# Optimization experiments

Hardware: AMD Instinct MI355X
Metric: run time of the kernel (lower is better)

## Reference

```python
import jax, jax.numpy as jnp
import numpy as np

N = 20000   # nodes
E = 320000  # edges (before self loops)
B = 32      # graphs in batch
H = 4       # heads
C = 64      # per-head channels
NEG_SLOPE = 0.2


def setup_inputs() -> dict:
    key = jax.random.key(0)
    ks = jax.random.split(key, 16)
    x = jax.random.normal(ks[0], (N, 62), jnp.float32)
    pos = jax.random.uniform(ks[1], (N, 2), jnp.float32)
    edge_index = jax.random.randint(ks[2], (2, E), 0, N, jnp.int64)
    batch = jnp.sort(jax.random.randint(ks[3], (N,), 0, B, jnp.int64))
    def glorot(k, shape):
        fan = shape[0] + shape[-1]
        return jax.random.normal(k, shape, jnp.float32) * jnp.sqrt(2.0 / fan)
    # GAT layer 1: in 64 -> H*C = 256
    W1 = glorot(ks[4], (64, H * C))
    a_src1 = glorot(ks[5], (H, C))
    a_dst1 = glorot(ks[6], (H, C))
    b1 = jnp.zeros((H * C,), jnp.float32)
    # GAT layer 2: in 256 -> 256
    W2 = glorot(ks[7], (H * C, H * C))
    a_src2 = glorot(ks[8], (H, C))
    a_dst2 = glorot(ks[9], (H, C))
    b2 = jnp.zeros((H * C,), jnp.float32)
    # linear tail 256 -> 128 -> 10
    lw1 = glorot(ks[10], (H * C, 128))
    lb1 = jnp.zeros((128,), jnp.float32)
    lw2 = glorot(ks[11], (128, 10))
    lb2 = jnp.zeros((10,), jnp.float32)
    return {"x": x, "pos": pos, "edge_index": edge_index, "batch": batch,
            "W1": W1, "a_src1": a_src1, "a_dst1": a_dst1, "b1": b1,
            "W2": W2, "a_src2": a_src2, "a_dst2": a_dst2, "b2": b2,
            "lw1": lw1, "lb1": lb1, "lw2": lw2, "lb2": lb2}


def gat_layer(x, src, dst, W, a_src, a_dst, b):
    # x: [N, F_in] -> h: [N, H, C]
    h = (x @ W).reshape(N, H, C)
    alpha_s = jnp.einsum('nhc,hc->nh', h, a_src)  # [N,H]
    alpha_d = jnp.einsum('nhc,hc->nh', h, a_dst)
    e = alpha_s[src] + alpha_d[dst]               # [E',H]
    e = jax.nn.leaky_relu(e, NEG_SLOPE)
    # softmax over incoming edges per destination node
    emax = jax.ops.segment_max(e, dst, num_segments=N)  # every node has a self loop
    p = jnp.exp(e - emax[dst])
    denom = jax.ops.segment_sum(p, dst, num_segments=N)
    alpha = p / (denom[dst] + 1e-16)              # [E',H]
    msg = h[src] * alpha[..., None]               # [E',H,C] gather + weight
    out = jax.ops.segment_sum(msg, dst, num_segments=N)  # scatter-add
    return out.reshape(N, H * C) + b


def reference(x, pos, edge_index, batch, W1, a_src1, a_dst1, b1,
              W2, a_src2, a_dst2, b2, lw1, lb1, lw2, lb2):
    out = jnp.concatenate([pos, x], axis=1)       # [N, 64]
    loop = jnp.arange(N, dtype=edge_index.dtype)
    src = jnp.concatenate([edge_index[0], loop])  # add self loops (PyG default)
    dst = jnp.concatenate([edge_index[1], loop])
    out = gat_layer(out, src, dst, W1, a_src1, a_dst1, b1)
    out = gat_layer(out, src, dst, W2, a_src2, a_dst2, b2)
    # global mean pool per graph
    sums = jax.ops.segment_sum(out, batch, num_segments=B)
    cnt = jax.ops.segment_sum(jnp.ones((N, 1), out.dtype), batch, num_segments=B)
    out = sums / jnp.maximum(cnt, 1.0)            # [B, 256]
    # dropout(p=0.2) is identity in eval mode
    out = jax.nn.relu(out @ lw1 + lb1)
    out = jax.nn.relu(out @ lw2 + lb2)            # relu after every linear, incl. last (faithful)
    return out
```

## Files before the change

kernel.cpp:

```cpp
#include <hip/hip_runtime.h>
#include <hip/hip_bf16.h>
#include <math.h>

#define N_NODES 20000
#define N_EDGES 320000
#define N_EDGES_SL (N_EDGES + N_NODES)
#define NB 32
#define NH 4
#define NC 64
#define HC 256
#define POOL_CH 20
#define DCAP 64

typedef short s16x8 __attribute__((ext_vector_type(8)));
typedef unsigned short u16x8 __attribute__((ext_vector_type(8)));
typedef float f32x4 __attribute__((ext_vector_type(4)));

__device__ __forceinline__ float bf2f(ushort u) {
    union { unsigned int i; float f; } v; v.i = ((unsigned int)u) << 16; return v.f;
}
__device__ __forceinline__ ushort f2bf(float f) {
    union { float f; unsigned int i; } v; v.f = f;
    unsigned int u = v.i;
    unsigned int r = (u + 0x7FFFu + ((u >> 16) & 1u)) >> 16;
    return (ushort)r;
}

#define PB_CONCAT 5000
#define PB_TCONV1 64
#define PB_TCONV2 256
#define PB_FILL   ((N_EDGES_SL + 255) / 256)
__global__ __launch_bounds__(256) void prep_kernel(const float* __restrict__ x,
                                                   const float* __restrict__ pos,
                                                   ushort* __restrict__ x0,
                                                   const float* __restrict__ W1,
                                                   ushort* __restrict__ Wt1,
                                                   const float* __restrict__ W2,
                                                   ushort* __restrict__ Wt2,
                                                   const int* __restrict__ ei,
                                                   int* __restrict__ fillc,
                                                   int* __restrict__ srclist,
                                                   const int* __restrict__ batch,
                                                   int* __restrict__ gstart) {
    int blk = blockIdx.x;
    if (blk < PB_CONCAT) {
        int i = blk * 256 + threadIdx.x;
        int n = i >> 6, j = i & 63;
        float v = (j < 2) ? pos[n * 2 + j] : x[n * 62 + (j - 2)];
        x0[i] = f2bf(v);
    } else if (blk < PB_CONCAT + PB_TCONV1) {
        int i = (blk - PB_CONCAT) * 256 + threadIdx.x;
        int n = i >> 6, k = i & 63;
        Wt1[i] = f2bf(W1[k * 256 + n]);
    } else if (blk < PB_CONCAT + PB_TCONV1 + PB_TCONV2) {
        int i = (blk - PB_CONCAT - PB_TCONV1) * 256 + threadIdx.x;
        int n = i >> 8, k = i & 255;
        Wt2[i] = f2bf(W2[k * 256 + n]);
    } else if (blk < PB_CONCAT + PB_TCONV1 + PB_TCONV2 + PB_FILL) {
        int i = (blk - PB_CONCAT - PB_TCONV1 - PB_TCONV2) * 256 + threadIdx.x;
        if (i >= N_EDGES_SL) return;
        int src, dst;
        if (i < N_EDGES) { src = ei[i]; dst = ei[N_EDGES + i]; }
        else             { src = i - N_EDGES; dst = src; }
        int slot = atomicAdd(&fillc[dst], 1);
        if (slot < DCAP) srclist[dst * DCAP + slot] = src;
    } else {
        int t = threadIdx.x;
        if (t > NB) return;
        int lo = 0, hi = N_NODES;
        while (lo < hi) {
            int mid = (lo + hi) >> 1;
            if (batch[mid] < t) lo = mid + 1; else hi = mid;
        }
        gstart[t] = lo;
    }
}

template<int K, int KC>
__global__ __launch_bounds__(256) void mfma_gemm(const ushort* __restrict__ A,
                                                 const ushort* __restrict__ Bt,
                                                 ushort* __restrict__ C,
                                                 const float* __restrict__ a_src,
                                                 const float* __restrict__ a_dst,
                                                 float* __restrict__ asb,
                                                 float* __restrict__ adb,
                                                 int M) {
    constexpr int KP = KC + 8;
    __shared__ __align__(16) ushort As[64 * KP];
    __shared__ __align__(16) ushort Bs[128 * KP];
    int tid = threadIdx.x;
    int row0 = blockIdx.y * 64, col0 = blockIdx.x * 128;
    int wave = tid >> 6, lane = tid & 63;
    int mm = lane & 15, quad = lane >> 4;
    f32x4 acc[8] = {};

    for (int kc0 = 0; kc0 < K; kc0 += KC) {
        if (kc0) __syncthreads();
        constexpr int ITER_A = (64 * KC) / 2048;
        constexpr int ITER_B = (128 * KC) / 2048;
#pragma unroll
        for (int it = 0; it < ITER_A; ++it) {
            int f = it * 2048 + tid * 8;
            int r = f / KC, k = f - r * KC;
            uint4 av = make_uint4(0u, 0u, 0u, 0u);
            if (row0 + r < M) av = *(const uint4*)&A[(size_t)(row0 + r) * K + kc0 + k];
            *(uint4*)&As[r * KP + k] = av;
        }
#pragma unroll
        for (int it = 0; it < ITER_B; ++it) {
            int f = it * 2048 + tid * 8;
            int r = f / KC, k = f - r * KC;
            uint4 bv = *(const uint4*)&Bt[(size_t)(col0 + r) * K + kc0 + k];
            *(uint4*)&Bs[r * KP + k] = bv;
        }
        __syncthreads();
#pragma unroll
        for (int kt = 0; kt < KC / 32; ++kt) {
            s16x8 a = *(const s16x8*)&As[(wave * 16 + mm) * KP + kt * 32 + quad * 8];
#pragma unroll
            for (int nt = 0; nt < 8; ++nt) {
                s16x8 b = *(const s16x8*)&Bs[(nt * 16 + mm) * KP + kt * 32 + quad * 8];
                acc[nt] = __builtin_amdgcn_mfma_f32_16x16x32_bf16(a, b, acc[nt], 0, 0, 0);
            }
        }
    }
#pragma unroll
    for (int r = 0; r < 4; ++r) {
        int gr = row0 + wave * 16 + quad * 4 + r;
        bool ok = gr < M;
        float s1a = 0.f, s2a = 0.f, s1b = 0.f, s2b = 0.f;
#pragma unroll
        for (int nt = 0; nt < 8; ++nt) {
            int gc = col0 + nt * 16 + mm;
            float av = acc[nt][r];
            if (ok) C[(size_t)gr * HC + gc] = f2bf(av);
            float as_ = a_src[gc], ad_ = a_dst[gc];
            if (nt < 4) { s1a += av * as_; s2a += av * ad_; }
            else        { s1b += av * as_; s2b += av * ad_; }
        }
#pragma unroll
        for (int off = 1; off < 16; off <<= 1) {
            s1a += __shfl_xor(s1a, off); s2a += __shfl_xor(s2a, off);
            s1b += __shfl_xor(s1b, off); s2b += __shfl_xor(s2b, off);
        }
        if (mm == 0 && ok) {
            int hd = col0 >> 6;
            asb[gr * NH + hd] = s1a;     adb[gr * NH + hd] = s2a;
            asb[gr * NH + hd + 1] = s1b; adb[gr * NH + hd + 1] = s2b;
        }
    }
}

__global__ __launch_bounds__(256) void gather_kernel(const ushort* __restrict__ h,
                                                     const float* __restrict__ as_in,
                                                     const float* __restrict__ ad_in,
                                                     const int* __restrict__ fillc,
                                                     const int* __restrict__ srclist,
                                                     const float* __restrict__ bias,
                                                     ushort* __restrict__ out) {
    __shared__ float wls[4][DCAP][NH];
    __shared__ int   sls[4][DCAP];
    __shared__ float dls[4][NH];
    int wave = threadIdx.x >> 6;
    int node = blockIdx.x * 4 + wave;
    int lane = threadIdx.x & 63;
    if (node >= N_NODES) return;
    int start = node * DCAP;
    int deg = fillc[node];

    {
        int hh = lane >> 4;
        int el = lane & 15;
        float adv = ad_in[node * NH + hh];
        float den = 0.f;
        for (int c = 0; c < deg; c += 16) {
            int j = c + el;
            if (j < deg) {
                int s = srclist[start + j];
                float e = as_in[s * NH + hh] + adv;
                e = (e > 0.f) ? e : 0.2f * e;
                float p = __expf(e);
                den += p;
                wls[wave][j][hh] = p;
                if (hh == 0) sls[wave][j] = s;
            }
        }
#pragma unroll
        for (int off = 8; off; off >>= 1) den += __shfl_xor(den, off);
        if (el == 0) dls[wave][hh] = den;
    }

    int ph = lane >> 5;
    int sl = lane & 31;
    int hh8 = sl >> 3;
    float invden = 1.0f / (dls[wave][hh8] + 1e-16f);
    float acc[8] = {0.f, 0.f, 0.f, 0.f, 0.f, 0.f, 0.f, 0.f};
#pragma unroll 4
    for (int j = 0; j < deg; j += 2) {
        int jj = j + ph;
        float p = 0.f;
        int s = 0;
        if (jj < deg) {
            s = sls[wave][jj];
            p = wls[wave][jj][hh8];
        }
        u16x8 hv = *(const u16x8*)&h[(size_t)s * HC + sl * 8];
#pragma unroll
        for (int k = 0; k < 8; ++k) acc[k] += p * bf2f(hv[k]);
    }
#pragma unroll
    for (int k = 0; k < 8; ++k) acc[k] += __shfl_xor(acc[k], 32);
    if (ph == 0) {
        const float* bp = &bias[sl * 8];
        u16x8 o;
#pragma unroll
        for (int k = 0; k < 8; ++k) o[k] = f2bf(acc[k] * invden + bp[k]);
        *(u16x8*)&out[(size_t)node * HC + sl * 8] = o;
    }
}

__global__ __launch_bounds__(256) void gpool_kernel(const ushort* __restrict__ o2,
                                                    const int* __restrict__ gstart,
                                                    float* __restrict__ poolsum) {
    int b = blockIdx.x / POOL_CH, chunk = blockIdx.x % POOL_CH;
    int c = threadIdx.x;
    int s = gstart[b], e = gstart[b + 1];
    int cnt = e - s;
    int per = (cnt + POOL_CH - 1) / POOL_CH;
    int ns = s + chunk * per;
    int ne = min(ns + per, e);
    if (ns >= ne) return;
    float acc = 0.f;
    for (int n = ns; n < ne; ++n) acc += bf2f(o2[(size_t)n * HC + c]);
    atomicAdd(&poolsum[b * HC + c], acc);
}

__global__ __launch_bounds__(128) void tail_kernel(const float* __restrict__ poolsum,
                                                   const int* __restrict__ gstart,
                                                   const float* __restrict__ lw1,
                                                   const float* __restrict__ lb1,
                                                   const float* __restrict__ lw2,
                                                   const float* __restrict__ lb2,
                                                   float* __restrict__ out) {
    __shared__ float pm[HC];
    __shared__ float hid[128];
    int b = blockIdx.x, t = threadIdx.x;
    int cnt = gstart[b + 1] - gstart[b];
    float inv = 1.0f / (float)max(cnt, 1);
    pm[t] = poolsum[b * HC + t] * inv;
    pm[t + 128] = poolsum[b * HC + t + 128] * inv;
    __syncthreads();
    float s = lb1[t];
    for (int c = 0; c < HC; ++c) s += pm[c] * lw1[c * 128 + t];
    hid[t] = fmaxf(s, 0.f);
    __syncthreads();
    if (t < 10) {
        float s2 = lb2[t];
        for (int k = 0; k < 128; ++k) s2 += hid[k] * lw2[k * 10 + t];
        out[b * 10 + t] = fmaxf(s2, 0.f);
    }
}

extern "C" void kernel_launch(void* const* d_in, const int* in_sizes, int n_in,
                              void* d_out, int out_size, void* d_ws, size_t ws_size,
                              hipStream_t stream) {
    const float* x      = (const float*)d_in[0];
    const float* pos    = (const float*)d_in[1];
    const int*   ei     = (const int*)d_in[2];
    const int*   batch  = (const int*)d_in[3];
    const float* W1     = (const float*)d_in[4];
    const float* a_src1 = (const float*)d_in[5];
    const float* a_dst1 = (const float*)d_in[6];
    const float* b1     = (const float*)d_in[7];
    const float* W2     = (const float*)d_in[8];
    const float* a_src2 = (const float*)d_in[9];
    const float* a_dst2 = (const float*)d_in[10];
    const float* b2     = (const float*)d_in[11];
    const float* lw1    = (const float*)d_in[12];
    const float* lb1    = (const float*)d_in[13];
    const float* lw2    = (const float*)d_in[14];
    const float* lb2    = (const float*)d_in[15];
    float* out = (float*)d_out;

    char* ws = (char*)d_ws;
    size_t off = 0;
    auto alloc = [&](size_t bytes) -> void* {
        void* p = ws + off;
        off = (off + bytes + 255) & ~(size_t)255;
        return p;
    };
    int*    fillc   = (int*)alloc(N_NODES * 4);
    float*  poolsum = (float*)alloc(NB * HC * 4);
    size_t zero_bytes = off;
    int*    srclist = (int*)alloc((size_t)N_NODES * DCAP * 4);
    int*    gstart  = (int*)alloc((NB + 1) * 4);
    ushort* x0      = (ushort*)alloc((size_t)N_NODES * 64 * 2);
    ushort* Wt1     = (ushort*)alloc(256 * 64 * 2);
    ushort* Wt2     = (ushort*)alloc(256 * 256 * 2);
    ushort* hbuf    = (ushort*)alloc((size_t)N_NODES * HC * 2);
    ushort* o1      = (ushort*)alloc((size_t)N_NODES * HC * 2);
    float*  asb     = (float*)alloc((size_t)N_NODES * NH * 4);
    float*  adb     = (float*)alloc((size_t)N_NODES * NH * 4);
    ushort* o2 = o1;

    hipMemsetAsync(d_ws, 0, zero_bytes, stream);

    prep_kernel<<<PB_CONCAT + PB_TCONV1 + PB_TCONV2 + PB_FILL + 1, 256, 0, stream>>>(
        x, pos, x0, W1, Wt1, W2, Wt2, ei, fillc, srclist, batch, gstart);

    dim3 ggrid(2, (N_NODES + 63) / 64);
    int ngrid = (N_NODES + 3) / 4;
    mfma_gemm<64, 64><<<ggrid, 256, 0, stream>>>(x0, Wt1, hbuf, a_src1, a_dst1, asb, adb, N_NODES);
    gather_kernel<<<ngrid, 256, 0, stream>>>(hbuf, asb, adb, fillc, srclist, b1, o1);
    mfma_gemm<256, 128><<<ggrid, 256, 0, stream>>>(o1, Wt2, hbuf, a_src2, a_dst2, asb, adb, N_NODES);
    gather_kernel<<<ngrid, 256, 0, stream>>>(hbuf, asb, adb, fillc, srclist, b2, o2);
    gpool_kernel<<<NB * POOL_CH, HC, 0, stream>>>(o2, gstart, poolsum);
    tail_kernel<<<NB, 128, 0, stream>>>(poolsum, gstart, lw1, lb1, lw2, lb2, out);
}
```

Baseline: 203.7 us.

## Fuse all GAT stages into one persistent cooperative kernel with grid syncs

Replaces the memset plus seven separate launches with a single persistent cooperative kernel. The stages (prep, edge fill, two GEMM+gather layers, pooling, tail MLP) are separated by grid-wide barriers, and blocks loop over work items in grid-stride fashion. The GEMM tile is shrunk to 64x64 with a fixed 64-wide K chunk so it fits shared memory and the occupancy target. This removes launch and inter-kernel gaps. In exchange it adds grid.sync costs, narrower GEMM tiles and possible occupancy limits from the register cap.

```diff
diff --git a/kernel.cpp b/kernel.cpp
--- a/kernel.cpp
+++ b/kernel.cpp
@@ -1,16 +1,18 @@
 #include <hip/hip_runtime.h>
+#include <hip/hip_cooperative_groups.h>
 #include <hip/hip_bf16.h>
 #include <math.h>
+
+namespace cg = cooperative_groups;
 
 #define N_NODES 20000
 #define N_EDGES 320000
 #define N_EDGES_SL (N_EDGES + N_NODES)
 #define NB 32
 #define NH 4
-#define NC 64
 #define HC 256
+#define DCAP 64
 #define POOL_CH 20
-#define DCAP 64
 
 typedef short s16x8 __attribute__((ext_vector_type(8)));
 typedef unsigned short u16x8 __attribute__((ext_vector_type(8)));
@@ -26,272 +28,267 @@
     return (ushort)r;
 }
 
+struct Params {
+    const float* x; const float* pos; const int* ei; const int* batch;
+    const float* W1; const float* a_src1; const float* a_dst1; const float* b1;
+    const float* W2; const float* a_src2; const float* a_dst2; const float* b2;
+    const float* lw1; const float* lb1; const float* lw2; const float* lb2;
+    float* out;
+    int* fillc; int* srclist; int* gstart;
+    ushort* x0; ushort* Wt1; ushort* Wt2; ushort* hbuf; ushort* o1;
+    float* asb; float* adb; float* poolsum;
+};
+
+template<int K>
+__device__ void gemm_phase(const ushort* __restrict__ A, const ushort* __restrict__ Bt,
+                           ushort* __restrict__ C,
+                           const float* __restrict__ a_src, const float* __restrict__ a_dst,
+                           float* __restrict__ asb, float* __restrict__ adb,
+                           char* smem) {
+    constexpr int KC = 64, KP = KC + 8;
+    ushort* As = (ushort*)smem;
+    ushort* Bs = (ushort*)(smem + 64 * KP * 2);
+    int tid = threadIdx.x;
+    int wave = tid >> 6, lane = tid & 63;
+    int mm = lane & 15, quad = lane >> 4;
+    const int TILES = 4 * ((N_NODES + 63) / 64);
+    for (int t = blockIdx.x; t < TILES; t += gridDim.x) {
+        int col0 = (t & 3) * 64;
+        int row0 = (t >> 2) * 64;
+        f32x4 acc[4] = {};
+        for (int kc0 = 0; kc0 < K; kc0 += KC) {
+            __syncthreads();
+#pragma unroll
+            for (int it = 0; it < 2; ++it) {
+                int f = it * 2048 + tid * 8;
+                int r = f >> 6, k = f & 63;
+                uint4 av = make_uint4(0u, 0u, 0u, 0u);
+                if (row0 + r < N_NODES) av = *(const uint4*)&A[(size_t)(row0 + r) * K + kc0 + k];
+                *(uint4*)&As[r * KP + k] = av;
+                uint4 bv = *(const uint4*)&Bt[(size_t)(col0 + r) * K + kc0 + k];
+                *(uint4*)&Bs[r * KP + k] = bv;
+            }
+            __syncthreads();
+#pragma unroll
+            for (int kt = 0; kt < KC / 32; ++kt) {
+                s16x8 a = *(const s16x8*)&As[(wave * 16 + mm) * KP + kt * 32 + quad * 8];
+#pragma unroll
+                for (int nt = 0; nt < 4; ++nt) {
+                    s16x8 b = *(const s16x8*)&Bs[(nt * 16 + mm) * KP + kt * 32 + quad * 8];
+                    acc[nt] = __builtin_amdgcn_mfma_f32_16x16x32_bf16(a, b, acc[nt], 0, 0, 0);
+                }
+            }
+        }
+        int hd = col0 >> 6;
+#pragma unroll
+        for (int r = 0; r < 4; ++r) {
+            int gr = row0 + wave * 16 + quad * 4 + r;
+            bool ok = gr < N_NODES;
+            float s1 = 0.f, s2 = 0.f;
+#pragma unroll
+            for (int nt = 0; nt < 4; ++nt) {
+                int gc = col0 + nt * 16 + mm;
+                float av = acc[nt][r];
+                if (ok) C[(size_t)gr * HC + gc] = f2bf(av);
+                s1 += av * a_src[gc];
+                s2 += av * a_dst[gc];
+            }
+#pragma unroll
+            for (int off = 1; off < 16; off <<= 1) {
+                s1 += __shfl_xor(s1, off);
+                s2 += __shfl_xor(s2, off);
+            }
+            if (mm == 0 && ok) { asb[gr * NH + hd] = s1; adb[gr * NH + hd] = s2; }
+        }
+    }
+}
+
+__device__ void gather_phase(const ushort* __restrict__ h,
+                             const float* __restrict__ as_in,
+                             const float* __restrict__ ad_in,
+                             const int* __restrict__ fillc,
+                             const int* __restrict__ srclist,
+                             const float* __restrict__ bias,
+                             ushort* __restrict__ out_,
+                             char* smem) {
+    float (*wls)[DCAP][NH] = (float (*)[DCAP][NH])smem;
+    int   (*sls)[DCAP]     = (int (*)[DCAP])(smem + 4096);
+    float (*dls)[NH]       = (float (*)[NH])(smem + 4096 + 1024);
+    int wave = threadIdx.x >> 6;
+    int lane = threadIdx.x & 63;
+    const int NGRP = (N_NODES + 3) / 4;
+    for (int grp = blockIdx.x; grp < NGRP; grp += gridDim.x) {
+        int node = grp * 4 + wave;
+        if (node < N_NODES) {
+            int start = node * DCAP;
+            int deg = fillc[node];
+            {
+                int hh = lane >> 4;
+                int el = lane & 15;
+                float adv = ad_in[node * NH + hh];
+                float den = 0.f;
+                for (int c = 0; c < deg; c += 16) {
+                    int j = c + el;
+                    if (j < deg) {
+                        int s = srclist[start + j];
+                        float e = as_in[s * NH + hh] + adv;
+                        e = (e > 0.f) ? e : 0.2f * e;
+                        float p = __expf(e);
+                        den += p;
+                        wls[wave][j][hh] = p;
+                        if (hh == 0) sls[wave][j] = s;
+                    }
+                }
+#pragma unroll
+                for (int off = 8; off; off >>= 1) den += __shfl_xor(den, off);
+                if (el == 0) dls[wave][hh] = den;
+            }
+            int ph = lane >> 5;
+            int sl = lane & 31;
+            int hh8 = sl >> 3;
+            float invden = 1.0f / (dls[wave][hh8] + 1e-16f);
+            float acc[8] = {0.f, 0.f, 0.f, 0.f, 0.f, 0.f, 0.f, 0.f};
+#pragma unroll 4
+            for (int j = 0; j < deg; j += 2) {
+                int jj = j + ph;
+                float p = 0.f;
+                int s = 0;
+                if (jj < deg) {
+                    s = sls[wave][jj];
+                    p = wls[wave][jj][hh8];
+                }
+                u16x8 hv = *(const u16x8*)&h[(size_t)s * HC + sl * 8];
+#pragma unroll
+                for (int k = 0; k < 8; ++k) acc[k] += p * bf2f(hv[k]);
+            }
+#pragma unroll
+            for (int k = 0; k < 8; ++k) acc[k] += __shfl_xor(acc[k], 32);
+            if (ph == 0) {
+                const float* bp = &bias[sl * 8];
+                u16x8 o;
+#pragma unroll
+                for (int k = 0; k < 8; ++k) o[k] = f2bf(acc[k] * invden + bp[k]);
+                *(u16x8*)&out_[(size_t)node * HC + sl * 8] = o;
+            }
+        }
+    }
+}
+
+#define PB_ZERO   ((N_NODES + NB * HC + 255) / 256)
 #define PB_CONCAT 5000
 #define PB_TCONV1 64
 #define PB_TCONV2 256
-#define PB_FILL   ((N_EDGES_SL + 255) / 256)
-__global__ __launch_bounds__(256) void prep_kernel(const float* __restrict__ x,
-                                                   const float* __restrict__ pos,
-                                                   ushort* __restrict__ x0,
-                                                   const float* __restrict__ W1,
-                                                   ushort* __restrict__ Wt1,
-                                                   const float* __restrict__ W2,
-                                                   ushort* __restrict__ Wt2,
-                                                   const int* __restrict__ ei,
-                                                   int* __restrict__ fillc,
-                                                   int* __restrict__ srclist,
-                                                   const int* __restrict__ batch,
-                                                   int* __restrict__ gstart) {
-    int blk = blockIdx.x;
-    if (blk < PB_CONCAT) {
-        int i = blk * 256 + threadIdx.x;
-        int n = i >> 6, j = i & 63;
-        float v = (j < 2) ? pos[n * 2 + j] : x[n * 62 + (j - 2)];
-        x0[i] = f2bf(v);
-    } else if (blk < PB_CONCAT + PB_TCONV1) {
-        int i = (blk - PB_CONCAT) * 256 + threadIdx.x;
-        int n = i >> 6, k = i & 63;
-        Wt1[i] = f2bf(W1[k * 256 + n]);
-    } else if (blk < PB_CONCAT + PB_TCONV1 + PB_TCONV2) {
-        int i = (blk - PB_CONCAT - PB_TCONV1) * 256 + threadIdx.x;
-        int n = i >> 8, k = i & 255;
-        Wt2[i] = f2bf(W2[k * 256 + n]);
-    } else if (blk < PB_CONCAT + PB_TCONV1 + PB_TCONV2 + PB_FILL) {
-        int i = (blk - PB_CONCAT - PB_TCONV1 - PB_TCONV2) * 256 + threadIdx.x;
-        if (i >= N_EDGES_SL) return;
-        int src, dst;
-        if (i < N_EDGES) { src = ei[i]; dst = ei[N_EDGES + i]; }
-        else             { src = i - N_EDGES; dst = src; }
-        int slot = atomicAdd(&fillc[dst], 1);
-        if (slot < DCAP) srclist[dst * DCAP + slot] = src;
-    } else {
-        int t = threadIdx.x;
-        if (t > NB) return;
-        int lo = 0, hi = N_NODES;
-        while (lo < hi) {
-            int mid = (lo + hi) >> 1;
-            if (batch[mid] < t) lo = mid + 1; else hi = mid;
-        }
-        gstart[t] = lo;
-    }
-}
-
-template<int K, int KC>
-__global__ __launch_bounds__(256) void mfma_gemm(const ushort* __restrict__ A,
-                                                 const ushort* __restrict__ Bt,
-                                                 ushort* __restrict__ C,
-                                                 const float* __restrict__ a_src,
-                                                 const float* __restrict__ a_dst,
-                                                 float* __restrict__ asb,
-                                                 float* __restrict__ adb,
-                                                 int M) {
-    constexpr int KP = KC + 8;
-    __shared__ __align__(16) ushort As[64 * KP];
-    __shared__ __align__(16) ushort Bs[128 * KP];
+#define P0_TOT (PB_ZERO + PB_CONCAT + PB_TCONV1 + PB_TCONV2 + 1)
+#define PB_FILL ((N_EDGES_SL + 255) / 256)
+
+__global__ __launch_bounds__(256, 4) void mega_kernel(Params p) {
+    __shared__ __align__(16) char smem[64 * 72 * 2 * 2];
+    cg::grid_group grid = cg::this_grid();
     int tid = threadIdx.x;
-    int row0 = blockIdx.y * 64, col0 = blockIdx.x * 128;
-    int wave = tid >> 6, lane = tid & 63;
-    int mm = lane & 15, quad = lane >> 4;
-    f32x4 acc[8] = {};
-
-    for (int kc0 = 0; kc0 < K; kc0 += KC) {
-        if (kc0) __syncthreads();
-        constexpr int ITER_A = (64 * KC) / 2048;
-        constexpr int ITER_B = (128 * KC) / 2048;
-#pragma unroll
-        for (int it = 0; it < ITER_A; ++it) {
-            int f = it * 2048 + tid * 8;
-            int r = f / KC, k = f - r * KC;
-            uint4 av = make_uint4(0u, 0u, 0u, 0u);
-            if (row0 + r < M) av = *(const uint4*)&A[(size_t)(row0 + r) * K + kc0 + k];
-            *(uint4*)&As[r * KP + k] = av;
-        }
-#pragma unroll
-        for (int it = 0; it < ITER_B; ++it) {
-            int f = it * 2048 + tid * 8;
-            int r = f / KC, k = f - r * KC;
-            uint4 bv = *(const uint4*)&Bt[(size_t)(col0 + r) * K + kc0 + k];
-            *(uint4*)&Bs[r * KP + k] = bv;
-        }
+
+    for (int blk = blockIdx.x; blk < P0_TOT; blk += gridDim.x) {
+        if (blk < PB_ZERO) {
+            int i = blk * 256 + tid;
+            if (i < N_NODES) p.fillc[i] = 0;
+            int j = i - N_NODES;
+            if (j >= 0 && j < NB * HC) p.poolsum[j] = 0.f;
+        } else if (blk < PB_ZERO + PB_CONCAT) {
+            int i = (blk - PB_ZERO) * 256 + tid;
+            int n = i >> 6, j = i & 63;
+            float v = (j < 2) ? p.pos[n * 2 + j] : p.x[n * 62 + (j - 2)];
+            p.x0[i] = f2bf(v);
+        } else if (blk < PB_ZERO + PB_CONCAT + PB_TCONV1) {
+            int i = (blk - PB_ZERO - PB_CONCAT) * 256 + tid;
+            int n = i >> 6, k = i & 63;
+            p.Wt1[i] = f2bf(p.W1[k * 256 + n]);
+        } else if (blk < PB_ZERO + PB_CONCAT + PB_TCONV1 + PB_TCONV2) {
+            int i = (blk - PB_ZERO - PB_CONCAT - PB_TCONV1) * 256 + tid;
+            int n = i >> 8, k = i & 255;
+            p.Wt2[i] = f2bf(p.W2[k * 256 + n]);
+        } else {
+            int t = tid;
+            if (t <= NB) {
+                int lo = 0, hi = N_NODES;
+                while (lo < hi) {
+                    int mid = (lo + hi) >> 1;
+                    if (p.batch[mid] < t) lo = mid + 1; else hi = mid;
+                }
+                p.gstart[t] = lo;
+            }
+        }
+    }
+    grid.sync();
+
+    for (int blk = blockIdx.x; blk < PB_FILL; blk += gridDim.x) {
+        int i = blk * 256 + tid;
+        if (i < N_EDGES_SL) {
+            int src, dst;
+            if (i < N_EDGES) { src = p.ei[i]; dst = p.ei[N_EDGES + i]; }
+            else             { src = i - N_EDGES; dst = src; }
+            int slot = atomicAdd(&p.fillc[dst], 1);
+            if (slot < DCAP) p.srclist[dst * DCAP + slot] = src;
+        }
+    }
+    grid.sync();
+
+    gemm_phase<64>(p.x0, p.Wt1, p.hbuf, p.a_src1, p.a_dst1, p.asb, p.adb, smem);
+    grid.sync();
+    gather_phase(p.hbuf, p.asb, p.adb, p.fillc, p.srclist, p.b1, p.o1, smem);
+    grid.sync();
+
+    gemm_phase<256>(p.o1, p.Wt2, p.hbuf, p.a_src2, p.a_dst2, p.asb, p.adb, smem);
+    grid.sync();
+    gather_phase(p.hbuf, p.asb, p.adb, p.fillc, p.srclist, p.b2, p.o1, smem);
+    grid.sync();
+
+    for (int c = blockIdx.x; c < NB * POOL_CH; c += gridDim.x) {
+        int b = c / POOL_CH, chunk = c % POOL_CH;
+        int s = p.gstart[b], e = p.gstart[b + 1];
+        int cnt = e - s;
+        int per = (cnt + POOL_CH - 1) / POOL_CH;
+        int ns = s + chunk * per, ne = min(ns + per, e);
+        if (ns < ne) {
+            float acc = 0.f;
+            for (int n = ns; n < ne; ++n) acc += bf2f(p.o1[(size_t)n * HC + tid]);
+            atomicAdd(&p.poolsum[b * HC + tid], acc);
+        }
+    }
+    grid.sync();
+
+    float* pm  = (float*)smem;
+    float* hid = (float*)(smem + 1024);
+    for (int b = blockIdx.x; b < NB; b += gridDim.x) {
+        int cnt = p.gstart[b + 1] - p.gstart[b];
+        float inv = 1.0f / (float)max(cnt, 1);
+        pm[tid] = p.poolsum[b * HC + tid] * inv;
         __syncthreads();
-#pragma unroll
-        for (int kt = 0; kt < KC / 32; ++kt) {
-            s16x8 a = *(const s16x8*)&As[(wave * 16 + mm) * KP + kt * 32 + quad * 8];
-#pragma unroll
-            for (int nt = 0; nt < 8; ++nt) {
-                s16x8 b = *(const s16x8*)&Bs[(nt * 16 + mm) * KP + kt * 32 + quad * 8];
-                acc[nt] = __builtin_amdgcn_mfma_f32_16x16x32_bf16(a, b, acc[nt], 0, 0, 0);
-            }
-        }
-    }
-#pragma unroll
-    for (int r = 0; r < 4; ++r) {
-        int gr = row0 + wave * 16 + quad * 4 + r;
-        bool ok = gr < M;
-        float s1a = 0.f, s2a = 0.f, s1b = 0.f, s2b = 0.f;
-#pragma unroll
-        for (int nt = 0; nt < 8; ++nt) {
-            int gc = col0 + nt * 16 + mm;
-            float av = acc[nt][r];
-            if (ok) C[(size_t)gr * HC + gc] = f2bf(av);
-            float as_ = a_src[gc], ad_ = a_dst[gc];
-            if (nt < 4) { s1a += av * as_; s2a += av * ad_; }
-            else        { s1b += av * as_; s2b += av * ad_; }
-        }
-#pragma unroll
-        for (int off = 1; off < 16; off <<= 1) {
-            s1a += __shfl_xor(s1a, off); s2a += __shfl_xor(s2a, off);
-            s1b += __shfl_xor(s1b, off); s2b += __shfl_xor(s2b, off);
-        }
-        if (mm == 0 && ok) {
-            int hd = col0 >> 6;
-            asb[gr * NH + hd] = s1a;     adb[gr * NH + hd] = s2a;
-            asb[gr * NH + hd + 1] = s1b; adb[gr * NH + hd + 1] = s2b;
-        }
-    }
-}
-
-__global__ __launch_bounds__(256) void gather_kernel(const ushort* __restrict__ h,
-                                                     const float* __restrict__ as_in,
-                                                     const float* __restrict__ ad_in,
-                                                     const int* __restrict__ fillc,
-                                                     const int* __restrict__ srclist,
-                                                     const float* __restrict__ bias,
-                                                     ushort* __restrict__ out) {
-    __shared__ float wls[4][DCAP][NH];
-    __shared__ int   sls[4][DCAP];
-    __shared__ float dls[4][NH];
-    int wave = threadIdx.x >> 6;
-    int node = blockIdx.x * 4 + wave;
-    int lane = threadIdx.x & 63;
-    if (node >= N_NODES) return;
-    int start = node * DCAP;
-    int deg = fillc[node];
-
-    {
-        int hh = lane >> 4;
-        int el = lane & 15;
-        float adv = ad_in[node * NH + hh];
-        float den = 0.f;
-        for (int c = 0; c < deg; c += 16) {
-            int j = c + el;
-            if (j < deg) {
-                int s = srclist[start + j];
-                float e = as_in[s * NH + hh] + adv;
-                e = (e > 0.f) ? e : 0.2f * e;
-                float p = __expf(e);
-                den += p;
-                wls[wave][j][hh] = p;
-                if (hh == 0) sls[wave][j] = s;
-            }
-        }
-#pragma unroll
-        for (int off = 8; off; off >>= 1) den += __shfl_xor(den, off);
-        if (el == 0) dls[wave][hh] = den;
-    }
-
-    int ph = lane >> 5;
-    int sl = lane & 31;
-    int hh8 = sl >> 3;
-    float invden = 1.0f / (dls[wave][hh8] + 1e-16f);
-    float acc[8] = {0.f, 0.f, 0.f, 0.f, 0.f, 0.f, 0.f, 0.f};
-#pragma unroll 4
-    for (int j = 0; j < deg; j += 2) {
-        int jj = j + ph;
-        float p = 0.f;
-        int s = 0;
-        if (jj < deg) {
-            s = sls[wave][jj];
-            p = wls[wave][jj][hh8];
-        }
-        u16x8 hv = *(const u16x8*)&h[(size_t)s * HC + sl * 8];
-#pragma unroll
-        for (int k = 0; k < 8; ++k) acc[k] += p * bf2f(hv[k]);
-    }
-#pragma unroll
-    for (int k = 0; k < 8; ++k) acc[k] += __shfl_xor(acc[k], 32);
-    if (ph == 0) {
-        const float* bp = &bias[sl * 8];
-        u16x8 o;
-#pragma unroll
-        for (int k = 0; k < 8; ++k) o[k] = f2bf(acc[k] * invden + bp[k]);
-        *(u16x8*)&out[(size_t)node * HC + sl * 8] = o;
-    }
-}
-
-__global__ __launch_bounds__(256) void gpool_kernel(const ushort* __restrict__ o2,
-                                                    const int* __restrict__ gstart,
-                                                    float* __restrict__ poolsum) {
-    int b = blockIdx.x / POOL_CH, chunk = blockIdx.x % POOL_CH;
-    int c = threadIdx.x;
-    int s = gstart[b], e = gstart[b + 1];
-    int cnt = e - s;
-    int per = (cnt + POOL_CH - 1) / POOL_CH;
-    int ns = s + chunk * per;
-    int ne = min(ns + per, e);
-    if (ns >= ne) return;
-    float acc = 0.f;
-    for (int n = ns; n < ne; ++n) acc += bf2f(o2[(size_t)n * HC + c]);
-    atomicAdd(&poolsum[b * HC + c], acc);
-}
-
-__global__ __launch_bounds__(128) void tail_kernel(const float* __restrict__ poolsum,
-                                                   const int* __restrict__ gstart,
-                                                   const float* __restrict__ lw1,
-                                                   const float* __restrict__ lb1,
-                                                   const float* __restrict__ lw2,
-                                                   const float* __restrict__ lb2,
-                                                   float* __restrict__ out) {
-    __shared__ float pm[HC];
-    __shared__ float hid[128];
-    int b = blockIdx.x, t = threadIdx.x;
-    int cnt = gstart[b + 1] - gstart[b];
-    float inv = 1.0f / (float)max(cnt, 1);
-    pm[t] = poolsum[b * HC + t] * inv;
-    pm[t + 128] = poolsum[b * HC + t + 128] * inv;
-    __syncthreads();
-    float s = lb1[t];
-    for (int c = 0; c < HC; ++c) s += pm[c] * lw1[c * 128 + t];
-    hid[t] = fmaxf(s, 0.f);
-    __syncthreads();
-    if (t < 10) {
-        float s2 = lb2[t];
-        for (int k = 0; k < 128; ++k) s2 += hid[k] * lw2[k * 10 + t];
-        out[b * 10 + t] = fmaxf(s2, 0.f);
+        if (tid < 128) {
+            float s = p.lb1[tid];
+            for (int c = 0; c < HC; ++c) s += pm[c] * p.lw1[c * 128 + tid];
+            hid[tid] = fmaxf(s, 0.f);
+        }
+        __syncthreads();
+        if (tid < 10) {
+            float s2 = p.lb2[tid];
+            for (int k = 0; k < 128; ++k) s2 += hid[k] * p.lw2[k * 10 + tid];
+            p.out[b * 10 + tid] = fmaxf(s2, 0.f);
+        }
+        __syncthreads();
     }
 }
 
 extern "C" void kernel_launch(void* const* d_in, const int* in_sizes, int n_in,
                               void* d_out, int out_size, void* d_ws, size_t ws_size,
                               hipStream_t stream) {
-    const float* x      = (const float*)d_in[0];
-    const float* pos    = (const float*)d_in[1];
-    const int*   ei     = (const int*)d_in[2];
-    const int*   batch  = (const int*)d_in[3];
-    const float* W1     = (const float*)d_in[4];
-    const float* a_src1 = (const float*)d_in[5];
-    const float* a_dst1 = (const float*)d_in[6];
-    const float* b1     = (const float*)d_in[7];
-    const float* W2     = (const float*)d_in[8];
-    const float* a_src2 = (const float*)d_in[9];
-    const float* a_dst2 = (const float*)d_in[10];
-    const float* b2     = (const float*)d_in[11];
-    const float* lw1    = (const float*)d_in[12];
-    const float* lb1    = (const float*)d_in[13];
-    const float* lw2    = (const float*)d_in[14];
-    const float* lb2    = (const float*)d_in[15];
-    float* out = (float*)d_out;
-
     char* ws = (char*)d_ws;
     size_t off = 0;
     auto alloc = [&](size_t bytes) -> void* {
-        void* p = ws + off;
+        void* pp = ws + off;
         off = (off + bytes + 255) & ~(size_t)255;
-        return p;
+        return pp;
     };
     int*    fillc   = (int*)alloc(N_NODES * 4);
     float*  poolsum = (float*)alloc(NB * HC * 4);
-    size_t zero_bytes = off;
     int*    srclist = (int*)alloc((size_t)N_NODES * DCAP * 4);
     int*    gstart  = (int*)alloc((NB + 1) * 4);
     ushort* x0      = (ushort*)alloc((size_t)N_NODES * 64 * 2);
@@ -301,19 +298,35 @@
     ushort* o1      = (ushort*)alloc((size_t)N_NODES * HC * 2);
     float*  asb     = (float*)alloc((size_t)N_NODES * NH * 4);
     float*  adb     = (float*)alloc((size_t)N_NODES * NH * 4);
-    ushort* o2 = o1;
-
-    hipMemsetAsync(d_ws, 0, zero_bytes, stream);
-
-    prep_kernel<<<PB_CONCAT + PB_TCONV1 + PB_TCONV2 + PB_FILL + 1, 256, 0, stream>>>(
-        x, pos, x0, W1, Wt1, W2, Wt2, ei, fillc, srclist, batch, gstart);
-
-    dim3 ggrid(2, (N_NODES + 63) / 64);
-    int ngrid = (N_NODES + 3) / 4;
-    mfma_gemm<64, 64><<<ggrid, 256, 0, stream>>>(x0, Wt1, hbuf, a_src1, a_dst1, asb, adb, N_NODES);
-    gather_kernel<<<ngrid, 256, 0, stream>>>(hbuf, asb, adb, fillc, srclist, b1, o1);
-    mfma_gemm<256, 128><<<ggrid, 256, 0, stream>>>(o1, Wt2, hbuf, a_src2, a_dst2, asb, adb, N_NODES);
-    gather_kernel<<<ngrid, 256, 0, stream>>>(hbuf, asb, adb, fillc, srclist, b2, o2);
-    gpool_kernel<<<NB * POOL_CH, HC, 0, stream>>>(o2, gstart, poolsum);
-    tail_kernel<<<NB, 128, 0, stream>>>(poolsum, gstart, lw1, lb1, lw2, lb2, out);
-}
+
+    Params p;
+    p.x      = (const float*)d_in[0];
+    p.pos    = (const float*)d_in[1];
+    p.ei     = (const int*)d_in[2];
+    p.batch  = (const int*)d_in[3];
+    p.W1     = (const float*)d_in[4];
+    p.a_src1 = (const float*)d_in[5];
+    p.a_dst1 = (const float*)d_in[6];
+    p.b1     = (const float*)d_in[7];
+    p.W2     = (const float*)d_in[8];
+    p.a_src2 = (const float*)d_in[9];
+    p.a_dst2 = (const float*)d_in[10];
+    p.b2     = (const float*)d_in[11];
+    p.lw1    = (const float*)d_in[12];
+    p.lb1    = (const float*)d_in[13];
+    p.lw2    = (const float*)d_in[14];
+    p.lb2    = (const float*)d_in[15];
+    p.out    = (float*)d_out;
+    p.fillc = fillc; p.srclist = srclist; p.gstart = gstart;
+    p.x0 = x0; p.Wt1 = Wt1; p.Wt2 = Wt2; p.hbuf = hbuf; p.o1 = o1;
+    p.asb = asb; p.adb = adb; p.poolsum = poolsum;
+
+    int maxb = 0;
+    hipOccupancyMaxActiveBlocksPerMultiprocessor(&maxb, mega_kernel, 256, 0);
+    if (maxb < 1) maxb = 1;
+    long grid = (long)maxb * 256;
+    if (grid > 2048) grid = 2048;
+
+    void* args[] = { (void*)&p };
+    hipLaunchCooperativeKernel(mega_kernel, dim3((unsigned)grid), dim3(256), args, 0, stream);
+}
```

Measured after the change: 686.2 us. 3.37x slower.

## Fold memset into prep, move edge fill into first GEMM, fuse pool and tail

Applied to the files above, without the earlier changes.

Replaces the workspace memset with zeroing blocks inside the prep kernel. The edge-bucketing fill moves out of prep and into extra blocks of the first GEMM launch, so it can overlap with the matrix multiply. The pooling and MLP tail kernels become one kernel, where the last-arriving block per graph (tracked with an atomic counter) runs the tail. This cuts two launches and one memset, at the cost of atomics and threadfences in the pool kernel.

```diff
diff --git a/kernel.cpp b/kernel.cpp
--- a/kernel.cpp
+++ b/kernel.cpp
@@ -7,7 +7,6 @@
 #define N_EDGES_SL (N_EDGES + N_NODES)
 #define NB 32
 #define NH 4
-#define NC 64
 #define HC 256
 #define POOL_CH 20
 #define DCAP 64
@@ -26,10 +25,11 @@
     return (ushort)r;
 }
 
+#define NZERO (N_NODES + NB * HC + NB)
+#define PB_ZERO   ((NZERO + 255) / 256)
 #define PB_CONCAT 5000
 #define PB_TCONV1 64
 #define PB_TCONV2 256
-#define PB_FILL   ((N_EDGES_SL + 255) / 256)
 __global__ __launch_bounds__(256) void prep_kernel(const float* __restrict__ x,
                                                    const float* __restrict__ pos,
                                                    ushort* __restrict__ x0,
@@ -37,33 +37,30 @@
                                                    ushort* __restrict__ Wt1,
                                                    const float* __restrict__ W2,
                                                    ushort* __restrict__ Wt2,
-                                                   const int* __restrict__ ei,
                                                    int* __restrict__ fillc,
-                                                   int* __restrict__ srclist,
+                                                   float* __restrict__ poolsum,
+                                                   int* __restrict__ done,
                                                    const int* __restrict__ batch,
                                                    int* __restrict__ gstart) {
     int blk = blockIdx.x;
-    if (blk < PB_CONCAT) {
+    if (blk < PB_ZERO) {
         int i = blk * 256 + threadIdx.x;
+        if (i < N_NODES) fillc[i] = 0;
+        else if (i < N_NODES + NB * HC) poolsum[i - N_NODES] = 0.f;
+        else if (i < NZERO) done[i - N_NODES - NB * HC] = 0;
+    } else if (blk < PB_ZERO + PB_CONCAT) {
+        int i = (blk - PB_ZERO) * 256 + threadIdx.x;
         int n = i >> 6, j = i & 63;
         float v = (j < 2) ? pos[n * 2 + j] : x[n * 62 + (j - 2)];
         x0[i] = f2bf(v);
-    } else if (blk < PB_CONCAT + PB_TCONV1) {
-        int i = (blk - PB_CONCAT) * 256 + threadIdx.x;
+    } else if (blk < PB_ZERO + PB_CONCAT + PB_TCONV1) {
+        int i = (blk - PB_ZERO - PB_CONCAT) * 256 + threadIdx.x;
         int n = i >> 6, k = i & 63;
         Wt1[i] = f2bf(W1[k * 256 + n]);
-    } else if (blk < PB_CONCAT + PB_TCONV1 + PB_TCONV2) {
-        int i = (blk - PB_CONCAT - PB_TCONV1) * 256 + threadIdx.x;
+    } else if (blk < PB_ZERO + PB_CONCAT + PB_TCONV1 + PB_TCONV2) {
+        int i = (blk - PB_ZERO - PB_CONCAT - PB_TCONV1) * 256 + threadIdx.x;
         int n = i >> 8, k = i & 255;
         Wt2[i] = f2bf(W2[k * 256 + n]);
-    } else if (blk < PB_CONCAT + PB_TCONV1 + PB_TCONV2 + PB_FILL) {
-        int i = (blk - PB_CONCAT - PB_TCONV1 - PB_TCONV2) * 256 + threadIdx.x;
-        if (i >= N_EDGES_SL) return;
-        int src, dst;
-        if (i < N_EDGES) { src = ei[i]; dst = ei[N_EDGES + i]; }
-        else             { src = i - N_EDGES; dst = src; }
-        int slot = atomicAdd(&fillc[dst], 1);
-        if (slot < DCAP) srclist[dst * DCAP + slot] = src;
     } else {
         int t = threadIdx.x;
         if (t > NB) return;
@@ -76,7 +73,8 @@
     }
 }
 
-template<int K, int KC>
+#define PB_FILL ((N_EDGES_SL + 255) / 256)
+template<int K, int KC, bool DOFILL>
 __global__ __launch_bounds__(256) void mfma_gemm(const ushort* __restrict__ A,
                                                  const ushort* __restrict__ Bt,
                                                  ushort* __restrict__ C,
@@ -84,12 +82,27 @@
                                                  const float* __restrict__ a_dst,
                                                  float* __restrict__ asb,
                                                  float* __restrict__ adb,
-                                                 int M) {
+                                                 const int* __restrict__ ei,
+                                                 int* __restrict__ fillc,
+                                                 int* __restrict__ srclist) {
     constexpr int KP = KC + 8;
+    constexpr int GEMM_BLOCKS = 2 * ((N_NODES + 63) / 64);
+    int t = blockIdx.x;
+    if (DOFILL && t >= GEMM_BLOCKS) {
+        int i = (t - GEMM_BLOCKS) * 256 + threadIdx.x;
+        if (i < N_EDGES_SL) {
+            int src, dst;
+            if (i < N_EDGES) { src = ei[i]; dst = ei[N_EDGES + i]; }
+            else             { src = i - N_EDGES; dst = src; }
+            int slot = atomicAdd(&fillc[dst], 1);
+            if (slot < DCAP) srclist[dst * DCAP + slot] = src;
+        }
+        return;
+    }
     __shared__ __align__(16) ushort As[64 * KP];
     __shared__ __align__(16) ushort Bs[128 * KP];
     int tid = threadIdx.x;
-    int row0 = blockIdx.y * 64, col0 = blockIdx.x * 128;
+    int col0 = (t & 1) * 128, row0 = (t >> 1) * 64;
     int wave = tid >> 6, lane = tid & 63;
     int mm = lane & 15, quad = lane >> 4;
     f32x4 acc[8] = {};
@@ -103,7 +116,7 @@
             int f = it * 2048 + tid * 8;
             int r = f / KC, k = f - r * KC;
             uint4 av = make_uint4(0u, 0u, 0u, 0u);
-            if (row0 + r < M) av = *(const uint4*)&A[(size_t)(row0 + r) * K + kc0 + k];
+            if (row0 + r < N_NODES) av = *(const uint4*)&A[(size_t)(row0 + r) * K + kc0 + k];
             *(uint4*)&As[r * KP + k] = av;
         }
 #pragma unroll
@@ -127,7 +140,7 @@
 #pragma unroll
     for (int r = 0; r < 4; ++r) {
         int gr = row0 + wave * 16 + quad * 4 + r;
-        bool ok = gr < M;
+        bool ok = gr < N_NODES;
         float s1a = 0.f, s2a = 0.f, s1b = 0.f, s2b = 0.f;
 #pragma unroll
         for (int nt = 0; nt < 8; ++nt) {
@@ -219,9 +232,18 @@
     }
 }
 
-__global__ __launch_bounds__(256) void gpool_kernel(const ushort* __restrict__ o2,
-                                                    const int* __restrict__ gstart,
-                                                    float* __restrict__ poolsum) {
+__global__ __launch_bounds__(256) void gpool_tail_kernel(const ushort* __restrict__ o2,
+                                                         const int* __restrict__ gstart,
+                                                         float* __restrict__ poolsum,
+                                                         int* __restrict__ done,
+                                                         const float* __restrict__ lw1,
+                                                         const float* __restrict__ lb1,
+                                                         const float* __restrict__ lw2,
+                                                         const float* __restrict__ lb2,
+                                                         float* __restrict__ out) {
+    __shared__ float pm[HC];
+    __shared__ float hid[128];
+    __shared__ int islast;
     int b = blockIdx.x / POOL_CH, chunk = blockIdx.x % POOL_CH;
     int c = threadIdx.x;
     int s = gstart[b], e = gstart[b + 1];
@@ -229,35 +251,33 @@
     int per = (cnt + POOL_CH - 1) / POOL_CH;
     int ns = s + chunk * per;
     int ne = min(ns + per, e);
-    if (ns >= ne) return;
-    float acc = 0.f;
-    for (int n = ns; n < ne; ++n) acc += bf2f(o2[(size_t)n * HC + c]);
-    atomicAdd(&poolsum[b * HC + c], acc);
-}
-
-__global__ __launch_bounds__(128) void tail_kernel(const float* __restrict__ poolsum,
-                                                   const int* __restrict__ gstart,
-                                                   const float* __restrict__ lw1,
-                                                   const float* __restrict__ lb1,
-                                                   const float* __restrict__ lw2,
-                                                   const float* __restrict__ lb2,
-                                                   float* __restrict__ out) {
-    __shared__ float pm[HC];
-    __shared__ float hid[128];
-    int b = blockIdx.x, t = threadIdx.x;
-    int cnt = gstart[b + 1] - gstart[b];
+    if (ns < ne) {
+        float acc = 0.f;
+        for (int n = ns; n < ne; ++n) acc += bf2f(o2[(size_t)n * HC + c]);
+        atomicAdd(&poolsum[b * HC + c], acc);
+    }
+    __threadfence();
+    __syncthreads();
+    if (c == 0) {
+        int old = atomicAdd(&done[b], 1);
+        islast = (old == POOL_CH - 1);
+    }
+    __syncthreads();
+    if (!islast) return;
+    __threadfence();
     float inv = 1.0f / (float)max(cnt, 1);
-    pm[t] = poolsum[b * HC + t] * inv;
-    pm[t + 128] = poolsum[b * HC + t + 128] * inv;
+    pm[c] = atomicAdd(&poolsum[b * HC + c], 0.0f) * inv;
     __syncthreads();
-    float s = lb1[t];
-    for (int c = 0; c < HC; ++c) s += pm[c] * lw1[c * 128 + t];
-    hid[t] = fmaxf(s, 0.f);
+    if (c < 128) {
+        float sacc = lb1[c];
+        for (int k = 0; k < HC; ++k) sacc += pm[k] * lw1[k * 128 + c];
+        hid[c] = fmaxf(sacc, 0.f);
+    }
     __syncthreads();
-    if (t < 10) {
-        float s2 = lb2[t];
-        for (int k = 0; k < 128; ++k) s2 += hid[k] * lw2[k * 10 + t];
-        out[b * 10 + t] = fmaxf(s2, 0.f);
+    if (c < 10) {
+        float s2 = lb2[c];
+        for (int k = 0; k < 128; ++k) s2 += hid[k] * lw2[k * 10 + c];
+        out[b * 10 + c] = fmaxf(s2, 0.f);
     }
 }
 
@@ -291,7 +311,7 @@
     };
     int*    fillc   = (int*)alloc(N_NODES * 4);
     float*  poolsum = (float*)alloc(NB * HC * 4);
-    size_t zero_bytes = off;
+    int*    done    = (int*)alloc(NB * 4);
     int*    srclist = (int*)alloc((size_t)N_NODES * DCAP * 4);
     int*    gstart  = (int*)alloc((NB + 1) * 4);
     ushort* x0      = (ushort*)alloc((size_t)N_NODES * 64 * 2);
@@ -303,17 +323,17 @@
     float*  adb     = (float*)alloc((size_t)N_NODES * NH * 4);
     ushort* o2 = o1;
 
-    hipMemsetAsync(d_ws, 0, zero_bytes, stream);
-
-    prep_kernel<<<PB_CONCAT + PB_TCONV1 + PB_TCONV2 + PB_FILL + 1, 256, 0, stream>>>(
-        x, pos, x0, W1, Wt1, W2, Wt2, ei, fillc, srclist, batch, gstart);
-
-    dim3 ggrid(2, (N_NODES + 63) / 64);
+    prep_kernel<<<PB_ZERO + PB_CONCAT + PB_TCONV1 + PB_TCONV2 + 1, 256, 0, stream>>>(
+        x, pos, x0, W1, Wt1, W2, Wt2, fillc, poolsum, done, batch, gstart);
+
+    const int GEMM_BLOCKS = 2 * ((N_NODES + 63) / 64);
     int ngrid = (N_NODES + 3) / 4;
-    mfma_gemm<64, 64><<<ggrid, 256, 0, stream>>>(x0, Wt1, hbuf, a_src1, a_dst1, asb, adb, N_NODES);
+    mfma_gemm<64, 64, true><<<GEMM_BLOCKS + PB_FILL, 256, 0, stream>>>(
+        x0, Wt1, hbuf, a_src1, a_dst1, asb, adb, ei, fillc, srclist);
     gather_kernel<<<ngrid, 256, 0, stream>>>(hbuf, asb, adb, fillc, srclist, b1, o1);
-    mfma_gemm<256, 128><<<ggrid, 256, 0, stream>>>(o1, Wt2, hbuf, a_src2, a_dst2, asb, adb, N_NODES);
+    mfma_gemm<256, 128, false><<<GEMM_BLOCKS, 256, 0, stream>>>(
+        o1, Wt2, hbuf, a_src2, a_dst2, asb, adb, ei, fillc, srclist);
     gather_kernel<<<ngrid, 256, 0, stream>>>(hbuf, asb, adb, fillc, srclist, b2, o2);
-    gpool_kernel<<<NB * POOL_CH, HC, 0, stream>>>(o2, gstart, poolsum);
-    tail_kernel<<<NB, 128, 0, stream>>>(poolsum, gstart, lw1, lb1, lw2, lb2, out);
-}
+    gpool_tail_kernel<<<NB * POOL_CH, HC, 0, stream>>>(o2, gstart, poolsum, done,
+                                                       lw1, lb1, lw2, lb2, out);
+}
```

Result: slower. 248.2 us (+21.8%).
